# Kernel tuning notes

Measured on AMD Instinct MI355X. Metric: run time of the kernel, lower is better.

## Reference

```python
import jax, jax.numpy as jnp
import numpy as np

N = 8192

def setup_inputs() -> dict:
    key = jax.random.key(0)
    k1, k2, k3, k4, k5, k6 = jax.random.split(key, 6)
    return {
        "t": jnp.zeros((), dtype=jnp.float32),
        "state": jax.random.uniform(k1, (3 * N,), dtype=jnp.float32),
        "betas": jax.random.uniform(k2, (N,), dtype=jnp.float32),
        "deltas": jax.random.uniform(k3, (N,), dtype=jnp.float32),
        "cs": jax.random.uniform(k4, (N,), dtype=jnp.float32),
        "ps": jax.random.uniform(k5, (N,), dtype=jnp.float32),
        "ts": jax.random.uniform(k6, (N, N), dtype=jnp.float32) * 0.5,
    }

def reference(t, state, betas, deltas, cs, ps, ts):
    # squared parametrization of all learned params
    T = jnp.square(ts)                      # [N, N]
    diag = jnp.diagonal(T)                  # T[n, n]
    row_sum = jnp.sum(T, axis=1)            # sum over T[n, :]
    # normalization[n] = min(T[n,n] / (sum_k T[n,k] - T[n,n]), 1)
    norm = jnp.minimum(diag / (row_sum - diag), jnp.float32(1.0))

    s = state.reshape(-1, 3)                # [N, 3] -> (U, I, V) per host
    U, I, V = s[:, 0], s[:, 1], s[:, 2]

    b2 = jnp.square(betas)
    d2 = jnp.square(deltas)
    p2 = jnp.square(ps)
    c2 = jnp.square(cs)

    bUV = b2 * U * V
    dU = -bUV
    dI = bUV - d2 * I
    # coupling[n] = sum_{nbr != n} norm[nbr] * T[nbr, n] * V[nbr]
    coupling = (norm * V) @ T - norm * diag * V
    dV = p2 * I - c2 * V - diag + coupling

    return jnp.stack([dU, dI, dV], axis=1).reshape(-1)
```

## Files before the change

kernel.cpp:

```cpp
#include <hip/hip_runtime.h>

#define NN 8192
#define CHUNKS 64
#define ROWS_PER_CHUNK (NN / CHUNKS)


__global__ void row_pass(const float* __restrict__ ts,
                         const float* __restrict__ state,
                         float* __restrict__ w,
                         float* __restrict__ diag_out) {
    const int row = blockIdx.x;
    const float4* rowp = reinterpret_cast<const float4*>(ts + (size_t)row * NN);
    float sum = 0.f;
    for (int k = threadIdx.x; k < NN / 4; k += 256) {
        float4 v = rowp[k];
        sum += v.x * v.x + v.y * v.y + v.z * v.z + v.w * v.w;
    }
    #pragma unroll
    for (int off = 32; off > 0; off >>= 1) sum += __shfl_down(sum, off);
    __shared__ float red[4];
    const int lane = threadIdx.x & 63;
    const int wid  = threadIdx.x >> 6;
    if (lane == 0) red[wid] = sum;
    __syncthreads();
    if (threadIdx.x == 0) {
        float total = red[0] + red[1] + red[2] + red[3];
        float d = ts[(size_t)row * NN + row];
        d = d * d;
        float norm = fminf(d / (total - d), 1.0f);
        float V = state[3 * row + 2];
        w[row] = norm * V;
        diag_out[row] = d;
    }
}

__global__ void col_pass(const float* __restrict__ ts,
                         const float* __restrict__ w,
                         float* __restrict__ partial) {
    const int colBase = blockIdx.x * 1024 + threadIdx.x * 4;
    const int row0 = blockIdx.y * ROWS_PER_CHUNK;
    float4 acc = {0.f, 0.f, 0.f, 0.f};
    const float* base = ts + (size_t)row0 * NN + colBase;
    #pragma unroll 4
    for (int r = 0; r < ROWS_PER_CHUNK; ++r) {
        const float wi = w[row0 + r];
        float4 v = *reinterpret_cast<const float4*>(base + (size_t)r * NN);
        acc.x += wi * v.x * v.x;
        acc.y += wi * v.y * v.y;
        acc.z += wi * v.z * v.z;
        acc.w += wi * v.w * v.w;
    }
    *reinterpret_cast<float4*>(partial + (size_t)blockIdx.y * NN + colBase) = acc;
}

__global__ void finalize(const float* __restrict__ state,
                         const float* __restrict__ betas,
                         const float* __restrict__ deltas,
                         const float* __restrict__ cs,
                         const float* __restrict__ ps,
                         const float* __restrict__ w,
                         const float* __restrict__ diag,
                         const float* __restrict__ partial,
                         float* __restrict__ out) {
    const int j = blockIdx.x * blockDim.x + threadIdx.x;
    if (j >= NN) return;
    float coup = 0.f;
    #pragma unroll 8
    for (int c = 0; c < CHUNKS; ++c) coup += partial[(size_t)c * NN + j];
    const float dj = diag[j];
    coup -= w[j] * dj;

    const float U = state[3 * j + 0];
    const float I = state[3 * j + 1];
    const float V = state[3 * j + 2];
    const float b2 = betas[j] * betas[j];
    const float d2 = deltas[j] * deltas[j];
    const float p2 = ps[j] * ps[j];
    const float c2 = cs[j] * cs[j];
    const float bUV = b2 * U * V;

    out[3 * j + 0] = -bUV;
    out[3 * j + 1] = bUV - d2 * I;
    out[3 * j + 2] = p2 * I - c2 * V - dj + coup;
}

extern "C" void kernel_launch(void* const* d_in, const int* in_sizes, int n_in,
                              void* d_out, int out_size, void* d_ws, size_t ws_size,
                              hipStream_t stream) {
    const float* state  = (const float*)d_in[1];
    const float* betas  = (const float*)d_in[2];
    const float* deltas = (const float*)d_in[3];
    const float* cs     = (const float*)d_in[4];
    const float* ps     = (const float*)d_in[5];
    const float* ts     = (const float*)d_in[6];
    float* out = (float*)d_out;

    float* w       = (float*)d_ws;
    float* diag    = w + NN;
    float* partial = diag + NN;

    row_pass<<<NN, 256, 0, stream>>>(ts, state, w, diag);

    dim3 g2(NN / 1024, CHUNKS);
    col_pass<<<g2, 256, 0, stream>>>(ts, w, partial);

    finalize<<<NN / 256, 256, 0, stream>>>(state, betas, deltas, cs, ps,
                                           w, diag, partial, out);
}
```

Before: 420.1 us.

## Fuse row, column and finalize passes into one cooperative kernel with grid syncs

```diff
diff --git a/kernel.cpp b/kernel.cpp
--- a/kernel.cpp
+++ b/kernel.cpp
@@ -1,87 +1,102 @@
 #include <hip/hip_runtime.h>
+#include <hip/hip_cooperative_groups.h>
+
+namespace cg = cooperative_groups;
 
 #define NN 8192
-#define CHUNKS 64
-#define ROWS_PER_CHUNK (NN / CHUNKS)
+#define NBLK 1024
+#define ROWS_PER_BLOCK (NN / NBLK)
+#define CHUNKS 128
+#define CHUNK_ROWS (NN / CHUNKS)
+#define COLTILES 8
 
 
-__global__ void row_pass(const float* __restrict__ ts,
-                         const float* __restrict__ state,
-                         float* __restrict__ w,
-                         float* __restrict__ diag_out) {
-    const int row = blockIdx.x;
-    const float4* rowp = reinterpret_cast<const float4*>(ts + (size_t)row * NN);
-    float sum = 0.f;
-    for (int k = threadIdx.x; k < NN / 4; k += 256) {
-        float4 v = rowp[k];
-        sum += v.x * v.x + v.y * v.y + v.z * v.z + v.w * v.w;
+__global__ void __launch_bounds__(256, 4)
+fused(const float* __restrict__ ts,
+      const float* __restrict__ state,
+      const float* __restrict__ betas,
+      const float* __restrict__ deltas,
+      const float* __restrict__ cs,
+      const float* __restrict__ ps,
+      float* __restrict__ w,
+      float* __restrict__ diag,
+      float* __restrict__ partial,
+      float* __restrict__ out)
+{
+    cg::grid_group grid = cg::this_grid();
+    const int tid  = threadIdx.x;
+    const int lane = tid & 63;
+    const int wid  = tid >> 6;
+
+    {
+        const int rowBase = blockIdx.x * ROWS_PER_BLOCK + wid * 2;
+        for (int r = 0; r < 2; ++r) {
+            const int row = rowBase + r;
+            const float4* rp = reinterpret_cast<const float4*>(ts + (size_t)row * NN);
+            float sum = 0.f;
+            #pragma unroll 8
+            for (int k = lane; k < NN / 4; k += 64) {
+                float4 v = rp[k];
+                sum += v.x * v.x + v.y * v.y + v.z * v.z + v.w * v.w;
+            }
+            #pragma unroll
+            for (int off = 32; off; off >>= 1) sum += __shfl_down(sum, off);
+            if (lane == 0) {
+                float d = ts[(size_t)row * NN + row];
+                d = d * d;
+                const float norm = fminf(d / (sum - d), 1.0f);
+                w[row]    = norm * state[3 * row + 2];
+                diag[row] = d;
+            }
+        }
     }
-    #pragma unroll
-    for (int off = 32; off > 0; off >>= 1) sum += __shfl_down(sum, off);
-    __shared__ float red[4];
-    const int lane = threadIdx.x & 63;
-    const int wid  = threadIdx.x >> 6;
-    if (lane == 0) red[wid] = sum;
-    __syncthreads();
-    if (threadIdx.x == 0) {
-        float total = red[0] + red[1] + red[2] + red[3];
-        float d = ts[(size_t)row * NN + row];
-        d = d * d;
-        float norm = fminf(d / (total - d), 1.0f);
-        float V = state[3 * row + 2];
-        w[row] = norm * V;
-        diag_out[row] = d;
+    grid.sync();
+
+    {
+        __shared__ float wsm[CHUNK_ROWS];
+        const int bx   = blockIdx.x & (COLTILES - 1);
+        const int by   = blockIdx.x >> 3;
+        const int row0 = by * CHUNK_ROWS;
+        if (tid < CHUNK_ROWS) wsm[tid] = w[row0 + tid];
+        __syncthreads();
+
+        const int col = bx * 1024 + tid * 4;
+        const float* base = ts + (size_t)row0 * NN + col;
+        float4 acc = {0.f, 0.f, 0.f, 0.f};
+        #pragma unroll 4
+        for (int r = 0; r < CHUNK_ROWS; ++r) {
+            const float wi = wsm[r];
+            float4 v = *reinterpret_cast<const float4*>(base + (size_t)r * NN);
+            acc.x += wi * v.x * v.x;
+            acc.y += wi * v.y * v.y;
+            acc.z += wi * v.z * v.z;
+            acc.w += wi * v.w * v.w;
+        }
+        *reinterpret_cast<float4*>(partial + (size_t)by * NN + col) = acc;
     }
-}
+    grid.sync();
 
-__global__ void col_pass(const float* __restrict__ ts,
-                         const float* __restrict__ w,
-                         float* __restrict__ partial) {
-    const int colBase = blockIdx.x * 1024 + threadIdx.x * 4;
-    const int row0 = blockIdx.y * ROWS_PER_CHUNK;
-    float4 acc = {0.f, 0.f, 0.f, 0.f};
-    const float* base = ts + (size_t)row0 * NN + colBase;
-    #pragma unroll 4
-    for (int r = 0; r < ROWS_PER_CHUNK; ++r) {
-        const float wi = w[row0 + r];
-        float4 v = *reinterpret_cast<const float4*>(base + (size_t)r * NN);
-        acc.x += wi * v.x * v.x;
-        acc.y += wi * v.y * v.y;
-        acc.z += wi * v.z * v.z;
-        acc.w += wi * v.w * v.w;
+    if (blockIdx.x < NN / 256) {
+        const int j = blockIdx.x * 256 + tid;
+        float coup = 0.f;
+        #pragma unroll 8
+        for (int c = 0; c < CHUNKS; ++c) coup += partial[(size_t)c * NN + j];
+        const float dj = diag[j];
+        coup -= w[j] * dj;
+
+        const float U = state[3 * j + 0];
+        const float I = state[3 * j + 1];
+        const float V = state[3 * j + 2];
+        const float b2 = betas[j] * betas[j];
+        const float d2 = deltas[j] * deltas[j];
+        const float p2 = ps[j] * ps[j];
+        const float c2 = cs[j] * cs[j];
+        const float bUV = b2 * U * V;
+
+        out[3 * j + 0] = -bUV;
+        out[3 * j + 1] = bUV - d2 * I;
+        out[3 * j + 2] = p2 * I - c2 * V - dj + coup;
     }
-    *reinterpret_cast<float4*>(partial + (size_t)blockIdx.y * NN + colBase) = acc;
-}
-
-__global__ void finalize(const float* __restrict__ state,
-                         const float* __restrict__ betas,
-                         const float* __restrict__ deltas,
-                         const float* __restrict__ cs,
-                         const float* __restrict__ ps,
-                         const float* __restrict__ w,
-                         const float* __restrict__ diag,
-                         const float* __restrict__ partial,
-                         float* __restrict__ out) {
-    const int j = blockIdx.x * blockDim.x + threadIdx.x;
-    if (j >= NN) return;
-    float coup = 0.f;
-    #pragma unroll 8
-    for (int c = 0; c < CHUNKS; ++c) coup += partial[(size_t)c * NN + j];
-    const float dj = diag[j];
-    coup -= w[j] * dj;
-
-    const float U = state[3 * j + 0];
-    const float I = state[3 * j + 1];
-    const float V = state[3 * j + 2];
-    const float b2 = betas[j] * betas[j];
-    const float d2 = deltas[j] * deltas[j];
-    const float p2 = ps[j] * ps[j];
-    const float c2 = cs[j] * cs[j];
-    const float bUV = b2 * U * V;
-
-    out[3 * j + 0] = -bUV;
-    out[3 * j + 1] = bUV - d2 * I;
-    out[3 * j + 2] = p2 * I - c2 * V - dj + coup;
 }
 
 extern "C" void kernel_launch(void* const* d_in, const int* in_sizes, int n_in,
@@ -99,11 +114,9 @@
     float* diag    = w + NN;
     float* partial = diag + NN;
 
-    row_pass<<<NN, 256, 0, stream>>>(ts, state, w, diag);
-
-    dim3 g2(NN / 1024, CHUNKS);
-    col_pass<<<g2, 256, 0, stream>>>(ts, w, partial);
-
-    finalize<<<NN / 256, 256, 0, stream>>>(state, betas, deltas, cs, ps,
-                                           w, diag, partial, out);
+    void* args[] = { (void*)&ts, (void*)&state, (void*)&betas, (void*)&deltas,
+                     (void*)&cs, (void*)&ps, (void*)&w, (void*)&diag,
+                     (void*)&partial, (void*)&out };
+    hipLaunchCooperativeKernel((const void*)fused, dim3(NBLK), dim3(256),
+                               args, 0, stream);
 }
```

After: 667.1 us. +58.8%, slower.
